# Kernel optimization log

Measured on AMD Instinct MI355X. Metric: run time of the kernel, lower is better.

## Reference

```python
import jax, jax.numpy as jnp
import numpy as np

B, H, N, D, RPE = 2, 8, 4096, 64, 64
LAYERS = 3


def _rms(x):
    # SimpleRMSNorm: x / sqrt(mean(x^2) + eps), no learned scale
    return x / jnp.sqrt(jnp.mean(x * x, axis=-1, keepdims=True) + 1e-8)


def setup_inputs() -> dict:
    key = jax.random.key(0)
    ks = jax.random.split(key, 7)
    s = 1.0 / np.sqrt(RPE)
    return {
        "x": jax.random.normal(ks[0], (B, H, N, D), dtype=jnp.float32),
        "w_in": jax.random.normal(ks[1], (1, RPE), dtype=jnp.float32) * 0.5,
        "b_in": jax.random.normal(ks[2], (RPE,), dtype=jnp.float32) * 0.02,
        "w_hid": jax.random.normal(ks[3], (LAYERS, RPE, RPE), dtype=jnp.float32) * s,
        "b_hid": jax.random.normal(ks[4], (LAYERS, RPE), dtype=jnp.float32) * 0.02,
        "w_out": jax.random.normal(ks[5], (RPE, H * D), dtype=jnp.float32) * s,
        "b_out": jax.random.normal(ks[6], (H * D,), dtype=jnp.float32) * 0.02,
    }


def reference(x, w_in, b_in, w_hid, b_hid, w_out, b_out):
    n = x.shape[-2]
    dt = x.dtype

    def rpe(idx):  # idx: (m, 1) relative-position features
        h = idx @ w_in + b_in  # (m, RPE)
        for i in range(LAYERS):  # non-residual: x = layer(x)
            h = jax.nn.relu(_rms(h)) @ w_hid[i] + b_hid[i]
        h = jax.nn.relu(_rms(h)) @ w_out + b_out  # (m, H*D)
        return h.reshape(-1, H, D).transpose(1, 0, 2)  # (H, m, D)

    zero_idx = jnp.ones((1, 1), dt)
    pos_idx = (1.0 / jnp.arange(2, n + 1, dtype=dt)).reshape(n - 1, 1)
    neg_idx = (-1.0 / jnp.arange(n, 1, -1, dtype=dt)).reshape(n - 1, 1)

    zero_k = rpe(zero_idx)  # (H, 1, D); used for both T[0] slots like the torch code
    a = jnp.concatenate([zero_k, rpe(pos_idx), zero_k, rpe(neg_idx)], axis=1)  # (H, 2n, D)
    # act_type='none' -> identity activation on a

    # Toeplitz matvec as circular conv of length 2n via FFT
    y = jnp.fft.rfft(x, 2 * n, axis=-2)          # (B, H, n+1, D) complex
    v = jnp.fft.rfft(a, 2 * n, axis=-2)[None]    # (1, H, n+1, D) complex
    out = jnp.fft.irfft(v * y, 2 * n, axis=-2)[:, :, :n, :]
    return out.astype(dt)
```

## Files before the change

### kernel.cpp

```cpp
#include <hip/hip_runtime.h>

#define N_SEQ 4096
#define N_FFT 8192
#define LAYERS 3
#define FT 512
#define PIDX(i) ((i) + ((i) >> 5))

template<int M>
__device__ inline void pass16_fwd(float* re, float* im, int tid)
{
    const int Q = M >> 4;
    const int j = tid & (Q - 1);
    const int G = tid / Q;
    const int base = G * M + j;
    const float KR[4] = {1.f, 0.9238795325f, 0.7071067812f, 0.3826834324f};
    const float KI[4] = {0.f, -0.3826834324f, -0.7071067812f, -0.9238795325f};
    float xr[4][4], xi[4][4];
#pragma unroll
    for (int a = 0; a < 4; ++a)
#pragma unroll
        for (int b = 0; b < 4; ++b) {
            int idx = PIDX(base + a * (M >> 2) + b * Q);
            xr[a][b] = re[idx]; xi[a][b] = im[idx];
        }
    float cj, sj;
    __sincosf(-6.283185307179586f / (float)M * (float)j, &sj, &cj);
#pragma unroll
    for (int b = 0; b < 4; ++b) {
        float c1 = cj * KR[b] - sj * KI[b];
        float s1 = cj * KI[b] + sj * KR[b];
        float c2 = c1 * c1 - s1 * s1, s2 = 2.f * c1 * s1;
        float c3 = c2 * c1 - s2 * s1, s3 = c2 * s1 + s2 * c1;
        float ar = xr[0][b] + xr[2][b], ai = xi[0][b] + xi[2][b];
        float br = xr[0][b] - xr[2][b], bi = xi[0][b] - xi[2][b];
        float cr = xr[1][b] + xr[3][b], ci = xi[1][b] + xi[3][b];
        float dr = xi[1][b] - xi[3][b], di = -(xr[1][b] - xr[3][b]);
        xr[0][b] = ar + cr;               xi[0][b] = ai + ci;
        float t1r = br + dr, t1i = bi + di;
        xr[1][b] = t1r * c1 - t1i * s1;   xi[1][b] = t1r * s1 + t1i * c1;
        float t2r = ar - cr, t2i = ai - ci;
        xr[2][b] = t2r * c2 - t2i * s2;   xi[2][b] = t2r * s2 + t2i * c2;
        float t3r = br - dr, t3i = bi - di;
        xr[3][b] = t3r * c3 - t3i * s3;   xi[3][b] = t3r * s3 + t3i * c3;
    }
    {
        float e1c = cj * cj - sj * sj, e1s = 2.f * cj * sj;
        float c1 = e1c * e1c - e1s * e1s, s1 = 2.f * e1c * e1s;
        float c2 = c1 * c1 - s1 * s1, s2 = 2.f * c1 * s1;
        float c3 = c2 * c1 - s2 * s1, s3 = c2 * s1 + s2 * c1;
#pragma unroll
        for (int a = 0; a < 4; ++a) {
            float ar = xr[a][0] + xr[a][2], ai = xi[a][0] + xi[a][2];
            float br = xr[a][0] - xr[a][2], bi = xi[a][0] - xi[a][2];
            float cr = xr[a][1] + xr[a][3], ci = xi[a][1] + xi[a][3];
            float dr = xi[a][1] - xi[a][3], di = -(xr[a][1] - xr[a][3]);
            xr[a][0] = ar + cr;               xi[a][0] = ai + ci;
            float t1r = br + dr, t1i = bi + di;
            xr[a][1] = t1r * c1 - t1i * s1;   xi[a][1] = t1r * s1 + t1i * c1;
            float t2r = ar - cr, t2i = ai - ci;
            xr[a][2] = t2r * c2 - t2i * s2;   xi[a][2] = t2r * s2 + t2i * c2;
            float t3r = br - dr, t3i = bi - di;
            xr[a][3] = t3r * c3 - t3i * s3;   xi[a][3] = t3r * s3 + t3i * c3;
        }
    }
#pragma unroll
    for (int a = 0; a < 4; ++a)
#pragma unroll
        for (int b = 0; b < 4; ++b) {
            int idx = PIDX(base + a * (M >> 2) + b * Q);
            re[idx] = xr[a][b]; im[idx] = xi[a][b];
        }
}

template<int M>
__device__ inline void pass16_inv(float* re, float* im, int tid)
{
    const int Q = M >> 4;
    const int j = tid & (Q - 1);
    const int G = tid / Q;
    const int base = G * M + j;
    const float KR[4] = {1.f, 0.9238795325f, 0.7071067812f, 0.3826834324f};
    const float KI[4] = {0.f, 0.3826834324f, 0.7071067812f, 0.9238795325f};
    float xr[4][4], xi[4][4];
#pragma unroll
    for (int a = 0; a < 4; ++a)
#pragma unroll
        for (int b = 0; b < 4; ++b) {
            int idx = PIDX(base + a * (M >> 2) + b * Q);
            xr[a][b] = re[idx]; xi[a][b] = im[idx];
        }
    float cj, sj;
    __sincosf(6.283185307179586f / (float)M * (float)j, &sj, &cj);
    {
        float e1c = cj * cj - sj * sj, e1s = 2.f * cj * sj;
        float c1 = e1c * e1c - e1s * e1s, s1 = 2.f * e1c * e1s;
        float c2 = c1 * c1 - s1 * s1, s2 = 2.f * c1 * s1;
        float c3 = c2 * c1 - s2 * s1, s3 = c2 * s1 + s2 * c1;
#pragma unroll
        for (int a = 0; a < 4; ++a) {
            float t0r = xr[a][0], t0i = xi[a][0];
            float t1r = xr[a][1] * c1 - xi[a][1] * s1, t1i = xr[a][1] * s1 + xi[a][1] * c1;
            float t2r = xr[a][2] * c2 - xi[a][2] * s2, t2i = xr[a][2] * s2 + xi[a][2] * c2;
            float t3r = xr[a][3] * c3 - xi[a][3] * s3, t3i = xr[a][3] * s3 + xi[a][3] * c3;
            float pr = t0r + t2r, pi = t0i + t2i;
            float qr = t0r - t2r, qi = t0i - t2i;
            float rr = t1r + t3r, ri = t1i + t3i;
            float sr = -(t1i - t3i), si = t1r - t3r;
            xr[a][0] = pr + rr; xi[a][0] = pi + ri;
            xr[a][1] = qr + sr; xi[a][1] = qi + si;
            xr[a][2] = pr - rr; xi[a][2] = pi - ri;
            xr[a][3] = qr - sr; xi[a][3] = qi - si;
        }
    }
#pragma unroll
    for (int b = 0; b < 4; ++b) {
        float c1 = cj * KR[b] - sj * KI[b];
        float s1 = cj * KI[b] + sj * KR[b];
        float c2 = c1 * c1 - s1 * s1, s2 = 2.f * c1 * s1;
        float c3 = c2 * c1 - s2 * s1, s3 = c2 * s1 + s2 * c1;
        float t0r = xr[0][b], t0i = xi[0][b];
        float t1r = xr[1][b] * c1 - xi[1][b] * s1, t1i = xr[1][b] * s1 + xi[1][b] * c1;
        float t2r = xr[2][b] * c2 - xi[2][b] * s2, t2i = xr[2][b] * s2 + xi[2][b] * c2;
        float t3r = xr[3][b] * c3 - xi[3][b] * s3, t3i = xr[3][b] * s3 + xi[3][b] * c3;
        float pr = t0r + t2r, pi = t0i + t2i;
        float qr = t0r - t2r, qi = t0i - t2i;
        float rr = t1r + t3r, ri = t1i + t3i;
        float sr = -(t1i - t3i), si = t1r - t3r;
        xr[0][b] = pr + rr; xi[0][b] = pi + ri;
        xr[1][b] = qr + sr; xi[1][b] = qi + si;
        xr[2][b] = pr - rr; xi[2][b] = pi - ri;
        xr[3][b] = qr - sr; xi[3][b] = qi - si;
    }
#pragma unroll
    for (int a = 0; a < 4; ++a)
#pragma unroll
        for (int b = 0; b < 4; ++b) {
            int idx = PIDX(base + a * (M >> 2) + b * Q);
            re[idx] = xr[a][b]; im[idx] = xi[a][b];
        }
}

__device__ inline void fwd8(float* zr, float* zi, int o)
{
    const float R = 0.70710678118654752f;
    {
        float ar = zr[o] + zr[o+4], ai = zi[o] + zi[o+4];
        float br = zr[o] - zr[o+4], bi = zi[o] - zi[o+4];
        float cr = zr[o+2] + zr[o+6], ci = zi[o+2] + zi[o+6];
        float dr = zi[o+2] - zi[o+6], di = -(zr[o+2] - zr[o+6]);
        zr[o]   = ar + cr; zi[o]   = ai + ci;
        zr[o+2] = br + dr; zi[o+2] = bi + di;
        zr[o+4] = ar - cr; zi[o+4] = ai - ci;
        zr[o+6] = br - dr; zi[o+6] = bi - di;
    }
    {
        float ar = zr[o+1] + zr[o+5], ai = zi[o+1] + zi[o+5];
        float br = zr[o+1] - zr[o+5], bi = zi[o+1] - zi[o+5];
        float cr = zr[o+3] + zr[o+7], ci = zi[o+3] + zi[o+7];
        float dr = zi[o+3] - zi[o+7], di = -(zr[o+3] - zr[o+7]);
        zr[o+1] = ar + cr; zi[o+1] = ai + ci;
        float t1r = br + dr, t1i = bi + di;
        zr[o+3] = R * (t1r + t1i); zi[o+3] = R * (t1i - t1r);
        float t2r = ar - cr, t2i = ai - ci;
        zr[o+5] = t2i;  zi[o+5] = -t2r;
        float t3r = br - dr, t3i = bi - di;
        zr[o+7] = R * (t3i - t3r); zi[o+7] = -R * (t3r + t3i);
    }
#pragma unroll
    for (int p = 0; p < 8; p += 2) {
        float ur = zr[o+p], ui = zi[o+p], vr = zr[o+p+1], vi = zi[o+p+1];
        zr[o+p]   = ur + vr; zi[o+p]   = ui + vi;
        zr[o+p+1] = ur - vr; zi[o+p+1] = ui - vi;
    }
}

__device__ inline void inv8(float* zr, float* zi, int o)
{
    const float R = 0.70710678118654752f;
#pragma unroll
    for (int p = 0; p < 8; p += 2) {
        float ur = zr[o+p], ui = zi[o+p], vr = zr[o+p+1], vi = zi[o+p+1];
        zr[o+p]   = ur + vr; zi[o+p]   = ui + vi;
        zr[o+p+1] = ur - vr; zi[o+p+1] = ui - vi;
    }
    {
        float t0r = zr[o],   t0i = zi[o];
        float t1r = zr[o+2], t1i = zi[o+2];
        float t2r = zr[o+4], t2i = zi[o+4];
        float t3r = zr[o+6], t3i = zi[o+6];
        float pr = t0r + t2r, pi = t0i + t2i;
        float qr = t0r - t2r, qi = t0i - t2i;
        float rr = t1r + t3r, ri = t1i + t3i;
        float sr = -(t1i - t3i), si = t1r - t3r;
        zr[o]   = pr + rr; zi[o]   = pi + ri;
        zr[o+2] = qr + sr; zi[o+2] = qi + si;
        zr[o+4] = pr - rr; zi[o+4] = pi - ri;
        zr[o+6] = qr - sr; zi[o+6] = qi - si;
    }
    {
        float t0r = zr[o+1], t0i = zi[o+1];
        float yr = zr[o+3], yi = zi[o+3];
        float t1r = R * (yr - yi), t1i = R * (yr + yi);
        yr = zr[o+5]; yi = zi[o+5];
        float t2r = -yi, t2i = yr;
        yr = zr[o+7]; yi = zi[o+7];
        float t3r = -R * (yr + yi), t3i = R * (yr - yi);
        float pr = t0r + t2r, pi = t0i + t2i;
        float qr = t0r - t2r, qi = t0i - t2i;
        float rr = t1r + t3r, ri = t1i + t3i;
        float sr = -(t1i - t3i), si = t1r - t3r;
        zr[o+1] = pr + rr; zi[o+1] = pi + ri;
        zr[o+3] = qr + sr; zi[o+3] = qi + si;
        zr[o+5] = pr - rr; zi[o+5] = pi - ri;
        zr[o+7] = qr - sr; zi[o+7] = qi - si;
    }
}

__global__ __launch_bounds__(256, 2) void prep_kernel(
    const float* __restrict__ x,
    const float* __restrict__ w_in, const float* __restrict__ b_in,
    const float* __restrict__ w_hid, const float* __restrict__ b_hid,
    const float* __restrict__ w_out, const float* __restrict__ b_out,
    float* __restrict__ a_t, float2* __restrict__ xt2)
{
    __shared__ __align__(16) char smem[33536];
    const int tid = threadIdx.x;

    if (blockIdx.x >= 256) {
        float (*t0)[65] = (float (*)[65])smem;
        float (*t1)[65] = (float (*)[65])(smem + 16640);
        int bb = blockIdx.x - 256;
        int h = bb >> 6;
        int nb = bb & 63;
        int lx = tid & 63;
        int ly = tid >> 6;
        const float* s0 = x + ((size_t)h * N_SEQ + nb * 64) * 64;
        const float* s1 = x + ((size_t)(8 + h) * N_SEQ + nb * 64) * 64;
        for (int r = ly; r < 64; r += 4) {
            t0[r][lx] = s0[r * 64 + lx];
            t1[r][lx] = s1[r * 64 + lx];
        }
        __syncthreads();
        for (int r = ly; r < 64; r += 4) {
            float2* dst = xt2 + (size_t)(h * 64 + r) * N_SEQ + nb * 64;
            dst[lx] = make_float2(t0[lx][r], t1[lx][r]);
        }
        return;
    }

    float (*ubuf)[36] = (float (*)[36])smem;
    float (*sums)[9]  = (float (*)[9])(smem + 9216);
    const int pos0 = blockIdx.x * 32;

    {
        const int p  = tid & 31;
        const int fp = tid >> 5;
        const int pos = pos0 + p;
        float v;
        if (pos == 0 || pos == N_SEQ) v = 1.0f;
        else if (pos < N_SEQ)         v = 1.0f / (float)(pos + 1);
        else                          v = -1.0f / (float)(2 * N_SEQ + 1 - pos);

        float h[8];
#pragma unroll
        for (int i = 0; i < 8; ++i) {
            int f = fp * 8 + i;
            h[i] = v * w_in[f] + b_in[f];
        }
        for (int L = 0; L <= LAYERS; ++L) {
            float s = 0.f;
#pragma unroll
            for (int i = 0; i < 8; ++i) s += h[i] * h[i];
            sums[p][fp] = s;
            __syncthreads();
            float tot = 0.f;
#pragma unroll
            for (int g = 0; g < 8; ++g) tot += sums[p][g];
            float r = rsqrtf(tot * (1.f / 64.f) + 1e-8f);
#pragma unroll
            for (int i = 0; i < 8; ++i)
                ubuf[fp * 8 + i][p] = fmaxf(h[i] * r, 0.f);
            __syncthreads();
            if (L == LAYERS) break;
            float acc[8];
#pragma unroll
            for (int i = 0; i < 8; ++i) acc[i] = b_hid[L * 64 + fp * 8 + i];
            const float* wb = w_hid + L * 4096 + fp * 8;
#pragma unroll 4
            for (int j = 0; j < 64; ++j) {
                float uj = ubuf[j][p];
                float4 w0 = *(const float4*)(wb + j * 64);
                float4 w1 = *(const float4*)(wb + j * 64 + 4);
                acc[0] = fmaf(uj, w0.x, acc[0]); acc[1] = fmaf(uj, w0.y, acc[1]);
                acc[2] = fmaf(uj, w0.z, acc[2]); acc[3] = fmaf(uj, w0.w, acc[3]);
                acc[4] = fmaf(uj, w1.x, acc[4]); acc[5] = fmaf(uj, w1.y, acc[5]);
                acc[6] = fmaf(uj, w1.z, acc[6]); acc[7] = fmaf(uj, w1.w, acc[7]);
            }
#pragma unroll
            for (int i = 0; i < 8; ++i) h[i] = acc[i];
        }
    }

    {
        const int p4 = tid & 7;
        const int of = tid >> 3;
        for (int co = 0; co < 4; ++co) {
            float acc[4][4];
#pragma unroll
            for (int i = 0; i < 4; ++i) {
                float bo = b_out[co * 128 + of * 4 + i];
#pragma unroll
                for (int k = 0; k < 4; ++k) acc[i][k] = bo;
            }
            const float* wb = w_out + co * 128 + of * 4;
#pragma unroll 4
            for (int j = 0; j < 64; ++j) {
                float4 u4 = *(const float4*)&ubuf[j][p4 * 4];
                float4 w4 = *(const float4*)(wb + j * 512);
                acc[0][0] = fmaf(u4.x, w4.x, acc[0][0]); acc[0][1] = fmaf(u4.y, w4.x, acc[0][1]);
                acc[0][2] = fmaf(u4.z, w4.x, acc[0][2]); acc[0][3] = fmaf(u4.w, w4.x, acc[0][3]);
                acc[1][0] = fmaf(u4.x, w4.y, acc[1][0]); acc[1][1] = fmaf(u4.y, w4.y, acc[1][1]);
                acc[1][2] = fmaf(u4.z, w4.y, acc[1][2]); acc[1][3] = fmaf(u4.w, w4.y, acc[1][3]);
                acc[2][0] = fmaf(u4.x, w4.z, acc[2][0]); acc[2][1] = fmaf(u4.y, w4.z, acc[2][1]);
                acc[2][2] = fmaf(u4.z, w4.z, acc[2][2]); acc[2][3] = fmaf(u4.w, w4.z, acc[2][3]);
                acc[3][0] = fmaf(u4.x, w4.w, acc[3][0]); acc[3][1] = fmaf(u4.y, w4.w, acc[3][1]);
                acc[3][2] = fmaf(u4.z, w4.w, acc[3][2]); acc[3][3] = fmaf(u4.w, w4.w, acc[3][3]);
            }
#pragma unroll
            for (int i = 0; i < 4; ++i) {
                float* dst = a_t + (size_t)(co * 128 + of * 4 + i) * N_FFT + pos0 + p4 * 4;
                *(float4*)dst = make_float4(acc[i][0], acc[i][1], acc[i][2], acc[i][3]);
            }
        }
    }
}

__global__ __launch_bounds__(FT, 2) void conv_kernel(const float* __restrict__ a_t,
                                                     const float2* __restrict__ xt2,
                                                     float2* __restrict__ out_t2)
{
    __shared__ float re[8448];
    __shared__ float im[8448];
    const int tid = threadIdx.x;
    const int hd = blockIdx.x;
    const float JR = 0.9238795325f;
    const float JI = -0.3826834324f;

    {
        const float* src = a_t + (size_t)hd * N_FFT;
        float ck, sk;
        __sincosf(-6.283185307179586f / 8192.f * (float)tid, &sk, &ck);
#pragma unroll
        for (int pp = 0; pp < 4; ++pp) {
            int k = pp * FT + tid;
            float x0 = src[k], x1 = src[k + 2048], x2 = src[k + 4096], x3 = src[k + 6144];
            float ar = x0 + x2, br = x0 - x2;
            float cr = x1 + x3, e = x1 - x3;
            re[PIDX(k)] = ar + cr; im[PIDX(k)] = 0.f;
            float c1 = ck, s1 = sk;
            float c2 = c1 * c1 - s1 * s1, s2 = 2.f * c1 * s1;
            float c3 = c2 * c1 - s2 * s1, s3 = c2 * s1 + s2 * c1;
            re[PIDX(k + 2048)] = br * c1 + e * s1;  im[PIDX(k + 2048)] = br * s1 - e * c1;
            float t2r = ar - cr;
            re[PIDX(k + 4096)] = t2r * c2;          im[PIDX(k + 4096)] = t2r * s2;
            re[PIDX(k + 6144)] = br * c3 - e * s3;  im[PIDX(k + 6144)] = br * s3 + e * c3;
            float tc = ck * JR - sk * JI; sk = ck * JI + sk * JR; ck = tc;
        }
    }
    __syncthreads();
    pass16_fwd<2048>(re, im, tid);
    __syncthreads();
    pass16_fwd<128>(re, im, tid);
    __syncthreads();
    float afr[16], afi[16];
    {
        const int base = tid * 16;
#pragma unroll
        for (int c = 0; c < 16; ++c) { int idx = PIDX(base + c); afr[c] = re[idx]; afi[c] = im[idx]; }
        fwd8(afr, afi, 0); fwd8(afr, afi, 8);
    }
    __syncthreads();
    {
        const float2* src = xt2 + (size_t)hd * N_SEQ;
        float ck, sk;
        __sincosf(-6.283185307179586f / 8192.f * (float)tid, &sk, &ck);
#pragma unroll
        for (int pp = 0; pp < 4; ++pp) {
            int k = pp * FT + tid;
            float2 z0 = src[k], z1 = src[k + 2048];
            float ar = z0.x, ai = z0.y;
            float cr = z1.x, ci = z1.y;
            float dr = z1.y, di = -z1.x;
            re[PIDX(k)] = ar + cr; im[PIDX(k)] = ai + ci;
            float c1 = ck, s1 = sk;
            float c2 = c1 * c1 - s1 * s1, s2 = 2.f * c1 * s1;
            float c3 = c2 * c1 - s2 * s1, s3 = c2 * s1 + s2 * c1;
            float t1r = ar + dr, t1i = ai + di;
            re[PIDX(k + 2048)] = t1r * c1 - t1i * s1; im[PIDX(k + 2048)] = t1r * s1 + t1i * c1;
            float t2r = ar - cr, t2i = ai - ci;
            re[PIDX(k + 4096)] = t2r * c2 - t2i * s2; im[PIDX(k + 4096)] = t2r * s2 + t2i * c2;
            float t3r = ar - dr, t3i = ai - di;
            re[PIDX(k + 6144)] = t3r * c3 - t3i * s3; im[PIDX(k + 6144)] = t3r * s3 + t3i * c3;
            float tc = ck * JR - sk * JI; sk = ck * JI + sk * JR; ck = tc;
        }
    }
    __syncthreads();
    pass16_fwd<2048>(re, im, tid);
    __syncthreads();
    pass16_fwd<128>(re, im, tid);
    __syncthreads();
    {
        const int base = tid * 16;
        float zr[16], zi[16];
#pragma unroll
        for (int c = 0; c < 16; ++c) { int idx = PIDX(base + c); zr[c] = re[idx]; zi[c] = im[idx]; }
        fwd8(zr, zi, 0); fwd8(zr, zi, 8);
        const float inv = 1.0f / (float)N_FFT;
#pragma unroll
        for (int c = 0; c < 16; ++c) {
            float xr = zr[c], xi_ = zi[c];
            zr[c] = (xr * afr[c] - xi_ * afi[c]) * inv;
            zi[c] = (xr * afi[c] + xi_ * afr[c]) * inv;
        }
        inv8(zr, zi, 0); inv8(zr, zi, 8);
#pragma unroll
        for (int c = 0; c < 16; ++c) { int idx = PIDX(base + c); re[idx] = zr[c]; im[idx] = zi[c]; }
    }
    __syncthreads();
    pass16_inv<128>(re, im, tid);
    __syncthreads();
    pass16_inv<2048>(re, im, tid);
    __syncthreads();
    {
        float2* dst = out_t2 + (size_t)hd * N_SEQ;
        float ck, sk;
        __sincosf(6.283185307179586f / 8192.f * (float)tid, &sk, &ck);
        const float JcR = 0.9238795325f, JcI = 0.3826834324f;
#pragma unroll
        for (int pp = 0; pp < 4; ++pp) {
            int k = pp * FT + tid;
            float c1 = ck, s1 = sk;
            float c2 = c1 * c1 - s1 * s1, s2 = 2.f * c1 * s1;
            float c3 = c2 * c1 - s2 * s1, s3 = c2 * s1 + s2 * c1;
            float t0r = re[PIDX(k)],        t0i = im[PIDX(k)];
            float y1r = re[PIDX(k + 2048)], y1i = im[PIDX(k + 2048)];
            float y2r = re[PIDX(k + 4096)], y2i = im[PIDX(k + 4096)];
            float y3r = re[PIDX(k + 6144)], y3i = im[PIDX(k + 6144)];
            float t1r = y1r * c1 - y1i * s1, t1i = y1r * s1 + y1i * c1;
            float t2r = y2r * c2 - y2i * s2, t2i = y2r * s2 + y2i * c2;
            float t3r = y3r * c3 - y3i * s3, t3i = y3r * s3 + y3i * c3;
            float pr = t0r + t2r, pi = t0i + t2i;
            float qr = t0r - t2r, qi = t0i - t2i;
            float rr = t1r + t3r, ri = t1i + t3i;
            float sr = -(t1i - t3i), si = t1r - t3r;
            dst[k]        = make_float2(pr + rr, pi + ri);
            dst[k + 2048] = make_float2(qr + sr, qi + si);
            float tc = ck * JcR - sk * JcI; sk = ck * JcI + sk * JcR; ck = tc;
        }
    }
}

__global__ __launch_bounds__(256) void transpose_o_kernel(const float2* __restrict__ out_t2,
                                                          float* __restrict__ out)
{
    __shared__ float t0[64][65];
    __shared__ float t1[64][65];
    int h = blockIdx.x >> 6;
    int nb = blockIdx.x & 63;
    int lx = threadIdx.x & 63;
    int ly = threadIdx.x >> 6;
    for (int r = ly; r < 64; r += 4) {
        float2 v = out_t2[(size_t)(h * 64 + r) * N_SEQ + nb * 64 + lx];
        t0[r][lx] = v.x;
        t1[r][lx] = v.y;
    }
    __syncthreads();
    float* d0 = out + ((size_t)h * N_SEQ + nb * 64) * 64;
    float* d1 = out + ((size_t)(8 + h) * N_SEQ + nb * 64) * 64;
    for (int r = ly; r < 64; r += 4) {
        d0[r * 64 + lx] = t0[lx][r];
        d1[r * 64 + lx] = t1[lx][r];
    }
}

extern "C" void kernel_launch(void* const* d_in, const int* in_sizes, int n_in,
                              void* d_out, int out_size, void* d_ws, size_t ws_size,
                              hipStream_t stream)
{
    const float* x     = (const float*)d_in[0];
    const float* w_in  = (const float*)d_in[1];
    const float* b_in  = (const float*)d_in[2];
    const float* w_hid = (const float*)d_in[3];
    const float* b_hid = (const float*)d_in[4];
    const float* w_out = (const float*)d_in[5];
    const float* b_out = (const float*)d_in[6];
    float* out = (float*)d_out;

    char* ws = (char*)d_ws;
    float2* xt2    = (float2*)ws;
    float*  a_t    = (float*)(ws + (size_t)16 * 1024 * 1024);
    float2* out_t2 = (float2*)(ws + (size_t)32 * 1024 * 1024);

    prep_kernel<<<768, 256, 0, stream>>>(x, w_in, b_in, w_hid, b_hid, w_out, b_out,
                                         a_t, xt2);
    conv_kernel<<<512, FT, 0, stream>>>(a_t, xt2, out_t2);
    transpose_o_kernel<<<512, 256, 0, stream>>>(out_t2, out);
}
```

Before: 159.5 us.

## Split prep work into more blocks and store x transpose as separate re/im planes

The RPE MLP blocks now split the output-projection column chunks across four blocks instead of looping over them, which recomputes the hidden MLP four times but quadruples parallelism. The x-transpose blocks now handle one batch each and write to separate real and imaginary planes instead of interleaved float2, halving shared memory per block to raise occupancy. The conv kernel reads the two planes with scalar loads. This trades redundant MLP compute and less vectorized loads for more blocks and better occupancy in the prep stage.

Measured after the change: 171.9 us. +7.7%, slower.

```diff
diff --git a/kernel.cpp b/kernel.cpp
--- a/kernel.cpp
+++ b/kernel.cpp
@@ -221,36 +221,34 @@
     const float* __restrict__ w_in, const float* __restrict__ b_in,
     const float* __restrict__ w_hid, const float* __restrict__ b_hid,
     const float* __restrict__ w_out, const float* __restrict__ b_out,
-    float* __restrict__ a_t, float2* __restrict__ xt2)
-{
-    __shared__ __align__(16) char smem[33536];
+    float* __restrict__ a_t, float* __restrict__ xt_re, float* __restrict__ xt_im)
+{
+    __shared__ __align__(16) char smem[16640];
     const int tid = threadIdx.x;
 
-    if (blockIdx.x >= 256) {
-        float (*t0)[65] = (float (*)[65])smem;
-        float (*t1)[65] = (float (*)[65])(smem + 16640);
-        int bb = blockIdx.x - 256;
-        int h = bb >> 6;
+    if (blockIdx.x >= 1024) {
+        float (*t)[65] = (float (*)[65])smem;
+        int bb = blockIdx.x - 1024;
+        int b  = bb >> 9;
+        int h  = (bb >> 6) & 7;
         int nb = bb & 63;
         int lx = tid & 63;
         int ly = tid >> 6;
-        const float* s0 = x + ((size_t)h * N_SEQ + nb * 64) * 64;
-        const float* s1 = x + ((size_t)(8 + h) * N_SEQ + nb * 64) * 64;
-        for (int r = ly; r < 64; r += 4) {
-            t0[r][lx] = s0[r * 64 + lx];
-            t1[r][lx] = s1[r * 64 + lx];
-        }
+        const float* src = x + ((size_t)(b * 8 + h) * N_SEQ + nb * 64) * 64;
+        float* plane = b ? xt_im : xt_re;
+        for (int r = ly; r < 64; r += 4)
+            t[r][lx] = src[r * 64 + lx];
         __syncthreads();
-        for (int r = ly; r < 64; r += 4) {
-            float2* dst = xt2 + (size_t)(h * 64 + r) * N_SEQ + nb * 64;
-            dst[lx] = make_float2(t0[lx][r], t1[lx][r]);
-        }
+        for (int r = ly; r < 64; r += 4)
+            plane[(size_t)(h * 64 + r) * N_SEQ + nb * 64 + lx] = t[lx][r];
         return;
     }
 
     float (*ubuf)[36] = (float (*)[36])smem;
     float (*sums)[9]  = (float (*)[9])(smem + 9216);
-    const int pos0 = blockIdx.x * 32;
+    const int pt = blockIdx.x >> 2;
+    const int co = blockIdx.x & 3;
+    const int pos0 = pt * 32;
 
     {
         const int p  = tid & 31;
@@ -304,39 +302,38 @@
     {
         const int p4 = tid & 7;
         const int of = tid >> 3;
-        for (int co = 0; co < 4; ++co) {
-            float acc[4][4];
-#pragma unroll
-            for (int i = 0; i < 4; ++i) {
-                float bo = b_out[co * 128 + of * 4 + i];
-#pragma unroll
-                for (int k = 0; k < 4; ++k) acc[i][k] = bo;
-            }
-            const float* wb = w_out + co * 128 + of * 4;
+        float acc[4][4];
+#pragma unroll
+        for (int i = 0; i < 4; ++i) {
+            float bo = b_out[co * 128 + of * 4 + i];
+#pragma unroll
+            for (int k = 0; k < 4; ++k) acc[i][k] = bo;
+        }
+        const float* wb = w_out + co * 128 + of * 4;
 #pragma unroll 4
-            for (int j = 0; j < 64; ++j) {
-                float4 u4 = *(const float4*)&ubuf[j][p4 * 4];
-                float4 w4 = *(const float4*)(wb + j * 512);
-                acc[0][0] = fmaf(u4.x, w4.x, acc[0][0]); acc[0][1] = fmaf(u4.y, w4.x, acc[0][1]);
-                acc[0][2] = fmaf(u4.z, w4.x, acc[0][2]); acc[0][3] = fmaf(u4.w, w4.x, acc[0][3]);
-                acc[1][0] = fmaf(u4.x, w4.y, acc[1][0]); acc[1][1] = fmaf(u4.y, w4.y, acc[1][1]);
-                acc[1][2] = fmaf(u4.z, w4.y, acc[1][2]); acc[1][3] = fmaf(u4.w, w4.y, acc[1][3]);
-                acc[2][0] = fmaf(u4.x, w4.z, acc[2][0]); acc[2][1] = fmaf(u4.y, w4.z, acc[2][1]);
-                acc[2][2] = fmaf(u4.z, w4.z, acc[2][2]); acc[2][3] = fmaf(u4.w, w4.z, acc[2][3]);
-                acc[3][0] = fmaf(u4.x, w4.w, acc[3][0]); acc[3][1] = fmaf(u4.y, w4.w, acc[3][1]);
-                acc[3][2] = fmaf(u4.z, w4.w, acc[3][2]); acc[3][3] = fmaf(u4.w, w4.w, acc[3][3]);
-            }
-#pragma unroll
-            for (int i = 0; i < 4; ++i) {
-                float* dst = a_t + (size_t)(co * 128 + of * 4 + i) * N_FFT + pos0 + p4 * 4;
-                *(float4*)dst = make_float4(acc[i][0], acc[i][1], acc[i][2], acc[i][3]);
-            }
+        for (int j = 0; j < 64; ++j) {
+            float4 u4 = *(const float4*)&ubuf[j][p4 * 4];
+            float4 w4 = *(const float4*)(wb + j * 512);
+            acc[0][0] = fmaf(u4.x, w4.x, acc[0][0]); acc[0][1] = fmaf(u4.y, w4.x, acc[0][1]);
+            acc[0][2] = fmaf(u4.z, w4.x, acc[0][2]); acc[0][3] = fmaf(u4.w, w4.x, acc[0][3]);
+            acc[1][0] = fmaf(u4.x, w4.y, acc[1][0]); acc[1][1] = fmaf(u4.y, w4.y, acc[1][1]);
+            acc[1][2] = fmaf(u4.z, w4.y, acc[1][2]); acc[1][3] = fmaf(u4.w, w4.y, acc[1][3]);
+            acc[2][0] = fmaf(u4.x, w4.z, acc[2][0]); acc[2][1] = fmaf(u4.y, w4.z, acc[2][1]);
+            acc[2][2] = fmaf(u4.z, w4.z, acc[2][2]); acc[2][3] = fmaf(u4.w, w4.z, acc[2][3]);
+            acc[3][0] = fmaf(u4.x, w4.w, acc[3][0]); acc[3][1] = fmaf(u4.y, w4.w, acc[3][1]);
+            acc[3][2] = fmaf(u4.z, w4.w, acc[3][2]); acc[3][3] = fmaf(u4.w, w4.w, acc[3][3]);
+        }
+#pragma unroll
+        for (int i = 0; i < 4; ++i) {
+            float* dst = a_t + (size_t)(co * 128 + of * 4 + i) * N_FFT + pos0 + p4 * 4;
+            *(float4*)dst = make_float4(acc[i][0], acc[i][1], acc[i][2], acc[i][3]);
         }
     }
 }
 
 __global__ __launch_bounds__(FT, 2) void conv_kernel(const float* __restrict__ a_t,
-                                                     const float2* __restrict__ xt2,
+                                                     const float* __restrict__ xt_re,
+                                                     const float* __restrict__ xt_im,
                                                      float2* __restrict__ out_t2)
 {
     __shared__ float re[8448];
@@ -381,16 +378,16 @@
     }
     __syncthreads();
     {
-        const float2* src = xt2 + (size_t)hd * N_SEQ;
+        const float* sre = xt_re + (size_t)hd * N_SEQ;
+        const float* sim = xt_im + (size_t)hd * N_SEQ;
         float ck, sk;
         __sincosf(-6.283185307179586f / 8192.f * (float)tid, &sk, &ck);
 #pragma unroll
         for (int pp = 0; pp < 4; ++pp) {
             int k = pp * FT + tid;
-            float2 z0 = src[k], z1 = src[k + 2048];
-            float ar = z0.x, ai = z0.y;
-            float cr = z1.x, ci = z1.y;
-            float dr = z1.y, di = -z1.x;
+            float ar = sre[k],        ai = sim[k];
+            float cr = sre[k + 2048], ci = sim[k + 2048];
+            float dr = ci, di = -cr;
             re[PIDX(k)] = ar + cr; im[PIDX(k)] = ai + ci;
             float c1 = ck, s1 = sk;
             float c2 = c1 * c1 - s1 * s1, s2 = 2.f * c1 * s1;
@@ -497,12 +494,13 @@
     float* out = (float*)d_out;
 
     char* ws = (char*)d_ws;
-    float2* xt2    = (float2*)ws;
+    float*  xt_re  = (float*)ws;
+    float*  xt_im  = (float*)(ws + (size_t)8 * 1024 * 1024);
     float*  a_t    = (float*)(ws + (size_t)16 * 1024 * 1024);
     float2* out_t2 = (float2*)(ws + (size_t)32 * 1024 * 1024);
 
-    prep_kernel<<<768, 256, 0, stream>>>(x, w_in, b_in, w_hid, b_hid, w_out, b_out,
-                                         a_t, xt2);
-    conv_kernel<<<512, FT, 0, stream>>>(a_t, xt2, out_t2);
+    prep_kernel<<<2048, 256, 0, stream>>>(x, w_in, b_in, w_hid, b_hid, w_out, b_out,
+                                          a_t, xt_re, xt_im);
+    conv_kernel<<<512, FT, 0, stream>>>(a_t, xt_re, xt_im, out_t2);
     transpose_o_kernel<<<512, 256, 0, stream>>>(out_t2, out);
 }
```
